# Kernel tuning notes

Measured on AMD Instinct MI355X. Metric: run time of the kernel, lower is better.

Reference implementation:

```python
import jax, jax.numpy as jnp
import numpy as np

B, T, I, H, O = 128, 512, 512, 2048, 512

def setup_inputs() -> dict:
    key = jax.random.key(0)
    ks = jax.random.split(key, 10)
    s = lambda fan_in: 1.0 / np.sqrt(fan_in)
    return {
        "x": jax.random.normal(ks[0], (B, T, I), dtype=jnp.float32),
        "dt": jnp.zeros((1,), dtype=jnp.float32),            # torch init: Tensor([0])
        "a": jnp.ones((1,), dtype=jnp.float32),              # torch init: Tensor([1])
        "enc_w": jax.random.uniform(ks[1], (H, I), jnp.float32, -s(I), s(I)),
        "enc_b": jax.random.uniform(ks[2], (H,), jnp.float32, -s(I), s(I)),
        "rec_w": jax.random.uniform(ks[3], (H, H), jnp.float32, -s(H), s(H)),
        "rec_b": jax.random.uniform(ks[4], (H,), jnp.float32, -s(H), s(H)),
        "dec_w": jax.random.uniform(ks[5], (O, H), jnp.float32, -s(H), s(H)),
        "dec_b": jax.random.uniform(ks[6], (O,), jnp.float32, -s(H), s(H)),
        "hi_w": jax.random.uniform(ks[7], (H, 1), jnp.float32, -1.0, 1.0),
        "hi_b": jax.random.uniform(ks[8], (H,), jnp.float32, -1.0, 1.0),
    }

def reference(x, dt, a, enc_w, enc_b, rec_w, rec_b, dec_w, dec_b, hi_w, hi_b):
    # x: [B, T, I] -> time-major [T, B, I]
    xt = jnp.transpose(x, (1, 0, 2))
    sdt = jax.nn.sigmoid(dt[0])          # scalar gate
    av = a[0]
    # hidden_init(ones(B,1)) = hi_w[:,0] + hi_b, broadcast over batch
    h0 = jnp.broadcast_to(hi_w[:, 0] + hi_b, (x.shape[0], hi_b.shape[0]))
    # precompute encoder projection for all timesteps: [T, B, H]
    enc = jnp.einsum('tbi,hi->tbh', xt, enc_w) + enc_b

    def step(h, e_t):
        h = (1.0 - sdt) * h + sdt * jnp.tanh(e_t + av * (h @ rec_w.T + rec_b))
        y = h @ dec_w.T + dec_b
        return h, y

    hidden, output = jax.lax.scan(step, h0, enc)
    return output, hidden
```

## Files before the change

### kernel.cpp

```cpp
#include <hip/hip_runtime.h>
#include <hip/hip_bf16.h>
#include <cmath>

#define Bb 128
#define Tt 512
#define Ii 512
#define Hh 2048
#define Oo 512
#define REC_GRID 256

typedef __bf16 bf16_t;
typedef __bf16 bf16x8 __attribute__((ext_vector_type(8)));
typedef __bf16 bf16x4 __attribute__((ext_vector_type(4)));
typedef float  f32x4_t __attribute__((ext_vector_type(4)));
typedef unsigned u32;

static __device__ __forceinline__ bf16_t to_b(float v){ return (bf16_t)v; }
static __device__ __forceinline__ float  b2f(unsigned short u){ unsigned x = ((unsigned)u)<<16; return __builtin_bit_cast(float, x); }
static __device__ __forceinline__ unsigned short f2bbits(float v){ return __builtin_bit_cast(unsigned short, to_b(v)); }

static __device__ __forceinline__ void gl_lds16(const void* g, void* l){
  __builtin_amdgcn_global_load_lds((const __attribute__((address_space(1))) void*)g,
                                   (__attribute__((address_space(3))) void*)l, 16, 0, 0);
}

#define REP8(M) M(0)M(1)M(2)M(3)M(4)M(5)M(6)M(7)

__global__ __launch_bounds__(256) void k_f2b(bf16_t* __restrict__ dst, const float* __restrict__ src){
  size_t i = ((size_t)blockIdx.x*256 + threadIdx.x)*4;
  float4 v = *(const float4*)(src + i);
  bf16x4 o; o[0]=to_b(v.x); o[1]=to_b(v.y); o[2]=to_b(v.z); o[3]=to_b(v.w);
  *(bf16x4*)(dst + i) = o;
}

__global__ __launch_bounds__(256) void k_init_h0(const float* __restrict__ hi_w, const float* __restrict__ hi_b,
                                                 bf16_t* __restrict__ h0b){
  int i = blockIdx.x*256 + threadIdx.x;
  bf16_t vb = to_b(hi_w[i] + hi_b[i]);
  for (int b=0;b<Bb;++b) h0b[(size_t)b*Hh + i] = vb;
}

__global__ __launch_bounds__(256) void k_convert_x(const float* __restrict__ x, bf16_t* __restrict__ x_tm){
  size_t idx = ((size_t)blockIdx.x*256 + threadIdx.x)*8;
  int    i0  = (int)(idx % Ii);
  size_t m   = idx / Ii;
  int    t   = (int)(m / Bb), b = (int)(m % Bb);
  const float* s = x + ((size_t)b*Tt + t)*Ii + i0;
  float4 v0 = *(const float4*)s, v1 = *(const float4*)(s+4);
  bf16x8 o;
  o[0]=to_b(v0.x); o[1]=to_b(v0.y); o[2]=to_b(v0.z); o[3]=to_b(v0.w);
  o[4]=to_b(v1.x); o[5]=to_b(v1.y); o[6]=to_b(v1.z); o[7]=to_b(v1.w);
  *(bf16x8*)(x_tm + idx) = o;
}

template<int ROWS, int KB>
static __device__ __forceinline__ void stage(const bf16_t* __restrict__ g, long ld, long row0, int k0,
                                             char* __restrict__ ldsT){
  constexpr int SLOTS = KB/8;
  constexpr int PT    = ROWS*SLOTS/256;
  #pragma unroll
  for (int j=0;j<PT;++j){
    int c    = threadIdx.x + 256*j;
    int row  = c / SLOTS, slot = c % SLOTS;
    uint4 v  = *(const uint4*)(g + (row0+row)*ld + k0 + slot*8);
    *(uint4*)(ldsT + row*(KB*2) + ((slot*16) ^ ((row&7)<<4))) = v;
  }
}

template<int KB>
static __device__ __forceinline__ bf16x8 frag(const char* __restrict__ ldsT, int row, int kk, int lane){
  int kbyte = kk*64 + ((lane>>4)<<4);
  return *(const bf16x8*)(ldsT + row*(KB*2) + (kbyte ^ ((row&7)<<4)));
}

template<int EPI>
__global__ __launch_bounds__(256) void gemm128(const bf16_t* __restrict__ A, long lda,
                                               const bf16_t* __restrict__ Bw, long ldb,
                                               const float* __restrict__ bias,
                                               void* __restrict__ Cout, long ldc, int K){
  constexpr int TM=128, TN=128, KB=64;
  __shared__ char lds[(TM+TN)*KB*2];
  char* ldsA = lds;
  char* ldsB = lds + TM*KB*2;
  long m0 = (long)blockIdx.x * TM;
  long n0 = (long)blockIdx.y * TN;
  int w = threadIdx.x >> 6, lane = threadIdx.x & 63;
  int wm = w >> 1, wn = w & 1;
  f32x4_t acc[4][4] = {};
  for (int k0=0;k0<K;k0+=KB){
    __syncthreads();
    stage<TM,KB>(A,  lda, m0, k0, ldsA);
    stage<TN,KB>(Bw, ldb, n0, k0, ldsB);
    __syncthreads();
    #pragma unroll
    for (int kk=0;kk<KB/32;++kk){
      bf16x8 af[4], bfv[4];
      #pragma unroll
      for (int f=0;f<4;++f){ int r = wm*64 + f*16 + (lane&15); af[f]  = frag<KB>(ldsA, r, kk, lane); }
      #pragma unroll
      for (int f=0;f<4;++f){ int r = wn*64 + f*16 + (lane&15); bfv[f] = frag<KB>(ldsB, r, kk, lane); }
      #pragma unroll
      for (int i=0;i<4;++i)
        #pragma unroll
        for (int j=0;j<4;++j)
          acc[i][j] = __builtin_amdgcn_mfma_f32_16x16x32_bf16(af[i], bfv[j], acc[i][j], 0,0,0);
    }
  }
  #pragma unroll
  for (int i=0;i<4;++i)
    #pragma unroll
    for (int j=0;j<4;++j)
      #pragma unroll
      for (int e=0;e<4;++e){
        long row = m0 + wm*64 + i*16 + ((lane>>4)<<2) + e;
        long col = n0 + wn*64 + j*16 + (lane&15);
        float v = acc[i][j][e] + bias[col];
        if (EPI==0) ((bf16_t*)Cout)[row*ldc + col] = to_b(v);
        else        ((float*) Cout)[row*ldc + col] = v;
      }
}

__global__ __launch_bounds__(512, 1) void rec_persist(
    const bf16_t* __restrict__ h0b, const bf16_t* __restrict__ W,
    bf16_t* __restrict__ EH, float* __restrict__ hfinal,
    const float* __restrict__ rec_b, const float* __restrict__ hi_w, const float* __restrict__ hi_b,
    const float* __restrict__ dtp, const float* __restrict__ ap,
    unsigned* __restrict__ flags)
{
  __shared__ char lds[131072];
  char* hbuf = lds;
  char* red  = lds + 65536;
  u32*  xb   = (u32*)(lds + 65536 + 32768);

  const int bid = blockIdx.x;
  const int g   = bid & 7;
  const int n   = bid >> 3;
  const int m0  = g * 16;
  const int n0  = n * 64;
  unsigned* gflags = flags + g*32*16;
  const int tid = threadIdx.x, w = tid >> 6, lane = tid & 63;
  const int l15 = lane & 15, w8 = w*8;

  #define WDCL(i) bf16x8 wa##i, wb##i, wc##i, wd##i;
  REP8(WDCL)
  #undef WDCL
  #pragma unroll 1
  for (int p = 0; p < 2; ++p){
    __syncthreads();
    for (int it = 0; it < 16; ++it){
      int cid = it*512 + tid;
      int lc  = cid & 63, kk = (cid >> 6) & 63, cgl = cid >> 12;
      uint4 v = *(const uint4*)(W + (size_t)(n0 + p*32 + cgl*16 + (lc&15))*Hh + kk*32 + ((lc>>4)<<3));
      *(uint4*)(lds + (size_t)cid*16) = v;
    }
    __syncthreads();
    if (p == 0){
      #define WRD0(i) \
        wa##i = *(const bf16x8*)(lds + (size_t)((     w8 + (i))*64 + lane)*16); \
        wb##i = *(const bf16x8*)(lds + (size_t)((64 + w8 + (i))*64 + lane)*16);
      REP8(WRD0)
      #undef WRD0
    } else {
      #define WRD1(i) \
        wc##i = *(const bf16x8*)(lds + (size_t)((     w8 + (i))*64 + lane)*16); \
        wd##i = *(const bf16x8*)(lds + (size_t)((64 + w8 + (i))*64 + lane)*16);
      REP8(WRD1)
      #undef WRD1
    }
  }
  __syncthreads();

  const float s  = 1.f/(1.f + __expf(-dtp[0]));
  const float av = ap[0];
  const int   cg_o = w & 3, eh = w >> 2;
  const int   batch = m0 + l15;
  const int   hcol0 = n0 + cg_o*16 + ((lane>>4)<<2) + eh*2;
  const int   lslot = l15*32 + cg_o*8 + (lane>>4)*2 + eh;
  float rb[2], hm[2];
  #pragma unroll
  for (int e=0;e<2;++e){ rb[e] = rec_b[hcol0+e]; hm[e] = hi_w[hcol0+e] + hi_b[hcol0+e]; }

  const size_t vsrc_off = (size_t)(m0 + l15)*Hh + ((lane>>4)<<3);
  const int co_b = m0 + (tid >> 5);
  const int co_c = n0 + (tid & 31)*2;
  const unsigned* fp = gflags + (w*4 + (lane & 3))*16;

  for (int t = 0; t < Tt; ++t){
    const bf16_t* Asrc = (t==0) ? h0b : (EH + (size_t)(t-1)*(Bb*Hh));
    bf16_t* EHt = EH + (size_t)t*(Bb*Hh);

    u32 ecv = __hip_atomic_load((const u32*)(EHt + (size_t)co_b*Hh + co_c),
                                __ATOMIC_RELAXED, __HIP_MEMORY_SCOPE_AGENT);

    if (t){
      unsigned tt = (unsigned)t;
      for (;;){
        unsigned v = __hip_atomic_load(fp, __ATOMIC_RELAXED, __HIP_MEMORY_SCOPE_AGENT);
        if (__all((int)(v >= tt))) break;
        __builtin_amdgcn_s_sleep(2);
      }
    }

    {
      const bf16_t* src = Asrc + vsrc_off;
      #pragma unroll
      for (int i = 0; i < 8; ++i)
        gl_lds16(src + (w8 + i)*32, hbuf + (size_t)(w8 + i)*1024);
    }
    asm volatile("s_waitcnt vmcnt(0)" ::: "memory");

    f32x4_t acc0 = {0.f,0.f,0.f,0.f}, acc1 = acc0, acc2 = acc0, acc3 = acc0;
    #define KS(i) { \
      bf16x8 hv = *(const bf16x8*)(hbuf + (size_t)(w8 + (i))*1024 + (size_t)lane*16); \
      acc0 = __builtin_amdgcn_mfma_f32_16x16x32_bf16(wa##i, hv, acc0, 0,0,0); \
      acc1 = __builtin_amdgcn_mfma_f32_16x16x32_bf16(wb##i, hv, acc1, 0,0,0); \
      acc2 = __builtin_amdgcn_mfma_f32_16x16x32_bf16(wc##i, hv, acc2, 0,0,0); \
      acc3 = __builtin_amdgcn_mfma_f32_16x16x32_bf16(wd##i, hv, acc3, 0,0,0); }
    REP8(KS)
    #undef KS

    *(f32x4_t*)(red + (size_t)((w*4 + 0)*64 + lane)*16) = acc0;
    *(f32x4_t*)(red + (size_t)((w*4 + 1)*64 + lane)*16) = acc1;
    *(f32x4_t*)(red + (size_t)((w*4 + 2)*64 + lane)*16) = acc2;
    *(f32x4_t*)(red + (size_t)((w*4 + 3)*64 + lane)*16) = acc3;
    xb[tid] = ecv;
    __syncthreads();
    f32x4_t fa = *(const f32x4_t*)(red + (size_t)((0*4 + cg_o)*64 + lane)*16);
    #pragma unroll
    for (int q=1;q<8;++q) fa = fa + *(const f32x4_t*)(red + (size_t)((q*4 + cg_o)*64 + lane)*16);

    u32 ev = xb[lslot];
    u32 ov = 0;
    #pragma unroll
    for (int e=0;e<2;++e){
      float enc = b2f((unsigned short)(ev >> (16*e)));
      float pre = enc + av*(fa[eh*2+e] + rb[e]);
      float th  = 1.f - 2.f/(__expf(2.f*pre) + 1.f);
      hm[e] = (1.f - s)*hm[e] + s*th;
      ov |= ((u32)f2bbits(hm[e])) << (16*e);
    }
    xb[lslot] = ov;
    __syncthreads();
    u32 hv = xb[tid];
    __hip_atomic_store((u32*)(EHt + (size_t)co_b*Hh + co_c), hv,
                       __ATOMIC_RELAXED, __HIP_MEMORY_SCOPE_AGENT);
    __syncthreads();
    if (tid == 0)
      __hip_atomic_store(gflags + n*16, (unsigned)(t+1),
                         __ATOMIC_RELAXED, __HIP_MEMORY_SCOPE_AGENT);
  }

  #pragma unroll
  for (int e=0;e<2;++e) hfinal[(size_t)batch*Hh + hcol0 + e] = hm[e];
}

extern "C" void kernel_launch(void* const* d_in, const int* in_sizes, int n_in,
                              void* d_out, int out_size, void* d_ws, size_t ws_size,
                              hipStream_t stream){
  const float* x     = (const float*)d_in[0];
  const float* dt    = (const float*)d_in[1];
  const float* a     = (const float*)d_in[2];
  const float* enc_w = (const float*)d_in[3];
  const float* enc_b = (const float*)d_in[4];
  const float* rec_w = (const float*)d_in[5];
  const float* rec_b = (const float*)d_in[6];
  const float* dec_w = (const float*)d_in[7];
  const float* dec_b = (const float*)d_in[8];
  const float* hi_w  = (const float*)d_in[9];
  const float* hi_b  = (const float*)d_in[10];
  float* out = (float*)d_out;

  char* ws = (char*)d_ws;
  size_t off = 0;
  auto carve = [&](size_t bytes)->char*{ char* p = ws + off; off += (bytes + 255) & ~(size_t)255; return p; };
  bf16_t* x_tm   = (bf16_t*)carve((size_t)Tt*Bb*Ii*2);
  bf16_t* EH     = (bf16_t*)carve((size_t)Tt*Bb*Hh*2);
  bf16_t* h0b    = (bf16_t*)carve((size_t)Bb*Hh*2);
  bf16_t* enc_wb = (bf16_t*)carve((size_t)Hh*Ii*2);
  bf16_t* rec_wb = (bf16_t*)carve((size_t)Hh*Hh*2);
  bf16_t* dec_wb = (bf16_t*)carve((size_t)Oo*Hh*2);
  unsigned* flags = (unsigned*)carve(8*32*16*4);
  if (off > ws_size) return;

  hipMemsetAsync(flags, 0, 8*32*16*4, stream);

  k_f2b<<<(Hh*Ii)/1024, 256, 0, stream>>>(enc_wb, enc_w);
  k_f2b<<<(Hh*Hh)/1024, 256, 0, stream>>>(rec_wb, rec_w);
  k_f2b<<<(Oo*Hh)/1024, 256, 0, stream>>>(dec_wb, dec_w);
  k_init_h0<<<Hh/256, 256, 0, stream>>>(hi_w, hi_b, h0b);
  k_convert_x<<<((size_t)Tt*Bb*Ii/8)/256, 256, 0, stream>>>(x, x_tm);

  gemm128<0><<<dim3((Tt*Bb)/128, Hh/128), 256, 0, stream>>>(x_tm, Ii, enc_wb, Ii, enc_b, EH, Hh, Ii);

  {
    float* hfinal = out + (size_t)Tt*Bb*Oo;
    void* args[] = { (void*)&h0b, (void*)&rec_wb, (void*)&EH, (void*)&hfinal,
                     (void*)&rec_b, (void*)&hi_w, (void*)&hi_b, (void*)&dt, (void*)&a,
                     (void*)&flags };
    hipLaunchCooperativeKernel((const void*)rec_persist, dim3(REC_GRID), dim3(512), args, 0, stream);
  }

  gemm128<1><<<dim3((Tt*Bb)/128, Oo/128), 256, 0, stream>>>(EH, Hh, dec_wb, Hh, dec_b, out, Oo, Hh);
}
```

Before: 2.638 ms.

## Split recurrent step K-dimension across 16 waves with 1024-thread blocks

```diff
diff --git a/kernel.cpp b/kernel.cpp
--- a/kernel.cpp
+++ b/kernel.cpp
@@ -24,7 +24,7 @@
                                    (__attribute__((address_space(3))) void*)l, 16, 0, 0);
 }
 
-#define REP8(M) M(0)M(1)M(2)M(3)M(4)M(5)M(6)M(7)
+#define REP4(M) M(0)M(1)M(2)M(3)
 
 __global__ __launch_bounds__(256) void k_f2b(bf16_t* __restrict__ dst, const float* __restrict__ src){
   size_t i = ((size_t)blockIdx.x*256 + threadIdx.x)*4;
@@ -120,17 +120,17 @@
       }
 }
 
-__global__ __launch_bounds__(512, 1) void rec_persist(
+__global__ __launch_bounds__(1024, 1) void rec_persist(
     const bf16_t* __restrict__ h0b, const bf16_t* __restrict__ W,
     bf16_t* __restrict__ EH, float* __restrict__ hfinal,
     const float* __restrict__ rec_b, const float* __restrict__ hi_w, const float* __restrict__ hi_b,
     const float* __restrict__ dtp, const float* __restrict__ ap,
     unsigned* __restrict__ flags)
 {
-  __shared__ char lds[131072];
-  char* hbuf = lds;
-  char* red  = lds + 65536;
-  u32*  xb   = (u32*)(lds + 65536 + 32768);
+  __shared__ char lds[65536 + 65536 + 4352];
+  char*  hbuf = lds;
+  float* redf = (float*)(lds + 65536);
+  float* xbf  = (float*)(lds + 131072);
 
   const int bid = blockIdx.x;
   const int g   = bid & 7;
@@ -139,58 +139,60 @@
   const int n0  = n * 64;
   unsigned* gflags = flags + g*32*16;
   const int tid = threadIdx.x, w = tid >> 6, lane = tid & 63;
-  const int l15 = lane & 15, w8 = w*8;
+  const int l15 = lane & 15, w4 = w*4;
 
   #define WDCL(i) bf16x8 wa##i, wb##i, wc##i, wd##i;
-  REP8(WDCL)
+  REP4(WDCL)
   #undef WDCL
   #pragma unroll 1
   for (int p = 0; p < 2; ++p){
     __syncthreads();
-    for (int it = 0; it < 16; ++it){
-      int cid = it*512 + tid;
+    for (int it = 0; it < 8; ++it){
+      int cid = it*1024 + tid;
       int lc  = cid & 63, kk = (cid >> 6) & 63, cgl = cid >> 12;
       uint4 v = *(const uint4*)(W + (size_t)(n0 + p*32 + cgl*16 + (lc&15))*Hh + kk*32 + ((lc>>4)<<3));
       *(uint4*)(lds + (size_t)cid*16) = v;
     }
     __syncthreads();
     if (p == 0){
-      #define WRD0(i) \
-        wa##i = *(const bf16x8*)(lds + (size_t)((     w8 + (i))*64 + lane)*16); \
-        wb##i = *(const bf16x8*)(lds + (size_t)((64 + w8 + (i))*64 + lane)*16);
-      REP8(WRD0)
-      #undef WRD0
+      #define WRD(i) \
+        wa##i = *(const bf16x8*)(lds + (size_t)((     w4 + (i))*64 + lane)*16); \
+        wb##i = *(const bf16x8*)(lds + (size_t)((64 + w4 + (i))*64 + lane)*16);
+      REP4(WRD)
+      #undef WRD
     } else {
-      #define WRD1(i) \
-        wc##i = *(const bf16x8*)(lds + (size_t)((     w8 + (i))*64 + lane)*16); \
-        wd##i = *(const bf16x8*)(lds + (size_t)((64 + w8 + (i))*64 + lane)*16);
-      REP8(WRD1)
-      #undef WRD1
+      #define WRD(i) \
+        wc##i = *(const bf16x8*)(lds + (size_t)((     w4 + (i))*64 + lane)*16); \
+        wd##i = *(const bf16x8*)(lds + (size_t)((64 + w4 + (i))*64 + lane)*16);
+      REP4(WRD)
+      #undef WRD
     }
   }
   __syncthreads();
 
   const float s  = 1.f/(1.f + __expf(-dtp[0]));
   const float av = ap[0];
-  const int   cg_o = w & 3, eh = w >> 2;
+  const int   cg_o = w & 3, eo = w >> 2;
   const int   batch = m0 + l15;
-  const int   hcol0 = n0 + cg_o*16 + ((lane>>4)<<2) + eh*2;
-  const int   lslot = l15*32 + cg_o*8 + (lane>>4)*2 + eh;
-  float rb[2], hm[2];
-  #pragma unroll
-  for (int e=0;e<2;++e){ rb[e] = rec_b[hcol0+e]; hm[e] = hi_w[hcol0+e] + hi_b[hcol0+e]; }
+  const int   col_l = cg_o*16 + ((lane >> 4) << 2) + eo;
+  const int   hcol  = n0 + col_l;
+  const int   pos   = l15*65 + col_l;
+  const float rbv = rec_b[hcol];
+  float hm = hi_w[hcol] + hi_b[hcol];
 
   const size_t vsrc_off = (size_t)(m0 + l15)*Hh + ((lane>>4)<<3);
   const int co_b = m0 + (tid >> 5);
   const int co_c = n0 + (tid & 31)*2;
-  const unsigned* fp = gflags + (w*4 + (lane & 3))*16;
+  const unsigned* fp = gflags + (w*2 + (lane & 1))*16;
 
   for (int t = 0; t < Tt; ++t){
     const bf16_t* Asrc = (t==0) ? h0b : (EH + (size_t)(t-1)*(Bb*Hh));
     bf16_t* EHt = EH + (size_t)t*(Bb*Hh);
 
-    u32 ecv = __hip_atomic_load((const u32*)(EHt + (size_t)co_b*Hh + co_c),
-                                __ATOMIC_RELAXED, __HIP_MEMORY_SCOPE_AGENT);
+    u32 ecv = 0;
+    if (tid < 512)
+      ecv = __hip_atomic_load((const u32*)(EHt + (size_t)co_b*Hh + co_c),
+                              __ATOMIC_RELAXED, __HIP_MEMORY_SCOPE_AGENT);
 
     if (t){
       unsigned tt = (unsigned)t;
@@ -204,54 +206,61 @@
     {
       const bf16_t* src = Asrc + vsrc_off;
       #pragma unroll
-      for (int i = 0; i < 8; ++i)
-        gl_lds16(src + (w8 + i)*32, hbuf + (size_t)(w8 + i)*1024);
+      for (int i = 0; i < 4; ++i)
+        gl_lds16(src + (w4 + i)*32, hbuf + (size_t)(w4 + i)*1024);
     }
     asm volatile("s_waitcnt vmcnt(0)" ::: "memory");
 
     f32x4_t acc0 = {0.f,0.f,0.f,0.f}, acc1 = acc0, acc2 = acc0, acc3 = acc0;
     #define KS(i) { \
-      bf16x8 hv = *(const bf16x8*)(hbuf + (size_t)(w8 + (i))*1024 + (size_t)lane*16); \
+      bf16x8 hv = *(const bf16x8*)(hbuf + (size_t)(w4 + (i))*1024 + (size_t)lane*16); \
       acc0 = __builtin_amdgcn_mfma_f32_16x16x32_bf16(wa##i, hv, acc0, 0,0,0); \
       acc1 = __builtin_amdgcn_mfma_f32_16x16x32_bf16(wb##i, hv, acc1, 0,0,0); \
       acc2 = __builtin_amdgcn_mfma_f32_16x16x32_bf16(wc##i, hv, acc2, 0,0,0); \
       acc3 = __builtin_amdgcn_mfma_f32_16x16x32_bf16(wd##i, hv, acc3, 0,0,0); }
-    REP8(KS)
+    REP4(KS)
     #undef KS
 
-    *(f32x4_t*)(red + (size_t)((w*4 + 0)*64 + lane)*16) = acc0;
-    *(f32x4_t*)(red + (size_t)((w*4 + 1)*64 + lane)*16) = acc1;
-    *(f32x4_t*)(red + (size_t)((w*4 + 2)*64 + lane)*16) = acc2;
-    *(f32x4_t*)(red + (size_t)((w*4 + 3)*64 + lane)*16) = acc3;
-    xb[tid] = ecv;
-    __syncthreads();
-    f32x4_t fa = *(const f32x4_t*)(red + (size_t)((0*4 + cg_o)*64 + lane)*16);
     #pragma unroll
-    for (int q=1;q<8;++q) fa = fa + *(const f32x4_t*)(red + (size_t)((q*4 + cg_o)*64 + lane)*16);
-
-    u32 ev = xb[lslot];
-    u32 ov = 0;
+    for (int e=0;e<4;++e){
+      redf[(w*16 +  0 + e)*64 + lane] = acc0[e];
+      redf[(w*16 +  4 + e)*64 + lane] = acc1[e];
+      redf[(w*16 +  8 + e)*64 + lane] = acc2[e];
+      redf[(w*16 + 12 + e)*64 + lane] = acc3[e];
+    }
+    if (tid < 512){
+      xbf[(tid>>5)*65 + (tid&31)*2    ] = b2f((unsigned short)(ecv & 0xffffu));
+      xbf[(tid>>5)*65 + (tid&31)*2 + 1] = b2f((unsigned short)(ecv >> 16));
+    }
+    __syncthreads();
+
+    float fa = 0.f;
     #pragma unroll
-    for (int e=0;e<2;++e){
-      float enc = b2f((unsigned short)(ev >> (16*e)));
-      float pre = enc + av*(fa[eh*2+e] + rb[e]);
+    for (int q=0;q<16;++q) fa += redf[(q*16 + cg_o*4 + eo)*64 + lane];
+
+    {
+      float enc = xbf[pos];
+      float pre = enc + av*(fa + rbv);
       float th  = 1.f - 2.f/(__expf(2.f*pre) + 1.f);
-      hm[e] = (1.f - s)*hm[e] + s*th;
-      ov |= ((u32)f2bbits(hm[e])) << (16*e);
-    }
-    xb[lslot] = ov;
-    __syncthreads();
-    u32 hv = xb[tid];
-    __hip_atomic_store((u32*)(EHt + (size_t)co_b*Hh + co_c), hv,
-                       __ATOMIC_RELAXED, __HIP_MEMORY_SCOPE_AGENT);
+      hm = (1.f - s)*hm + s*th;
+      xbf[pos] = hm;
+    }
+    __syncthreads();
+
+    if (tid < 512){
+      float h0f = xbf[(tid>>5)*65 + (tid&31)*2];
+      float h1f = xbf[(tid>>5)*65 + (tid&31)*2 + 1];
+      u32 ov = (u32)f2bbits(h0f) | ((u32)f2bbits(h1f) << 16);
+      __hip_atomic_store((u32*)(EHt + (size_t)co_b*Hh + co_c), ov,
+                         __ATOMIC_RELAXED, __HIP_MEMORY_SCOPE_AGENT);
+    }
     __syncthreads();
     if (tid == 0)
       __hip_atomic_store(gflags + n*16, (unsigned)(t+1),
                          __ATOMIC_RELAXED, __HIP_MEMORY_SCOPE_AGENT);
   }
 
-  #pragma unroll
-  for (int e=0;e<2;++e) hfinal[(size_t)batch*Hh + hcol0 + e] = hm[e];
+  hfinal[(size_t)batch*Hh + hcol] = hm;
 }
 
 extern "C" void kernel_launch(void* const* d_in, const int* in_sizes, int n_in,
@@ -297,7 +306,7 @@
     void* args[] = { (void*)&h0b, (void*)&rec_wb, (void*)&EH, (void*)&hfinal,
                      (void*)&rec_b, (void*)&hi_w, (void*)&hi_b, (void*)&dt, (void*)&a,
                      (void*)&flags };
-    hipLaunchCooperativeKernel((const void*)rec_persist, dim3(REC_GRID), dim3(512), args, 0, stream);
+    hipLaunchCooperativeKernel((const void*)rec_persist, dim3(REC_GRID), dim3(1024), args, 0, stream);
   }
 
   gemm128<1><<<dim3((Tt*Bb)/128, Oo/128), 256, 0, stream>>>(EH, Hh, dec_wb, Hh, dec_b, out, Oo, Hh);
```

Measured after the change: 2.406 ms (median of 2 runs). 1.1x faster.
